# Optimization experiments

Hardware: AMD Instinct MI355X
Metric: run time of the kernel (lower is better)

Reference implementation:

```python
import jax, jax.numpy as jnp
import numpy as np

N, SD, HD, CD, AD = 8192, 64, 128, 32, 8  # num_agents, state_dim, hidden_dim, comm_dim, action_dim
NOISE_SCALE = 0.01


def _l2norm(x, axis):
    # F.normalize: x / max(||x||_2, eps), eps=1e-12
    return x / jnp.maximum(jnp.linalg.norm(x, axis=axis, keepdims=True), 1e-12)


def setup_inputs() -> dict:
    key = jax.random.key(0)
    ks = jax.random.split(key, 12)
    def w(k, shape, scale=0.05):
        return jax.random.normal(k, shape, jnp.float32) * scale
    return {
        "states": jax.random.normal(ks[0], (N, SD), jnp.float32),
        "noise": jax.random.normal(ks[1], (N, HD), jnp.float32),
        # ReasoningCore: Linear(SD+CD->HD), ReLU, Linear(HD->HD)
        "W1": w(ks[2], (SD + CD, HD)), "b1": jnp.zeros((HD,), jnp.float32),
        "W2": w(ks[3], (HD, HD)),      "b2": jnp.zeros((HD,), jnp.float32),
        # CommunicationModule encoder: Linear(HD->CD)
        "Wc": w(ks[4], (HD, CD)), "bc": jnp.zeros((CD,), jnp.float32),
        # GNNLayer: Linear(HD->HD)
        "Wg": w(ks[5], (HD, HD)), "bg": jnp.zeros((HD,), jnp.float32),
        # Policy: Linear(HD->AD)
        "Wp": w(ks[6], (HD, AD)), "bp": jnp.zeros((AD,), jnp.float32),
        # Value: Linear(HD->1)
        "Wv": w(ks[7], (HD, 1)), "bv": jnp.zeros((1,), jnp.float32),
        # RoleHead: Linear(HD->3)
        "Wr": w(ks[8], (HD, 3)), "br": jnp.zeros((3,), jnp.float32),
    }


def reference(states, noise, W1, b1, W2, b2, Wc, bc, Wg, bg, Wp, bp, Wv, bv, Wr, br):
    def core(x, comm):
        h = jax.nn.relu(jnp.concatenate([x, comm], axis=-1) @ W1 + b1)  # [N, HD]
        return h @ W2 + b2

    comm0 = jnp.zeros((N, CD), states.dtype)
    H = core(states, comm0)                                   # [N, HD]
    msgs = _l2norm(H @ Wc + bc, axis=1)                       # [N, CD]
    comm = jnp.broadcast_to(msgs.mean(axis=0, keepdims=True), (N, CD))
    H = core(states, comm)                                    # [N, HD]
    adj = jnp.ones((N, N), states.dtype) / N                  # dense uniform adjacency
    H = jax.nn.relu((adj @ H) @ Wg + bg)                      # GNN layer
    H = _l2norm(H + noise * NOISE_SCALE, axis=1)
    actions = jnp.tanh(H @ Wp + bp)                           # [N, AD]
    values = H @ Wv + bv                                      # [N, 1]
    role_probs = jax.nn.softmax(H @ Wr + br, axis=-1)         # [N, 3]
    return (H, actions, values, role_probs)
```

## Files before the change

kernel.cpp:

```cpp
#include <hip/hip_runtime.h>
#include <math.h>

#define N_AG 8192
#define SD 64
#define HD 128
#define CD 32
#define AD 8

#define P_OFF     0
#define W2CT_OFF  (N_AG*HD)
#define WALLT_OFF (W2CT_OFF + CD*HD)
#define BALL_OFF  (WALLT_OFF + 12*HD)
#define BCP_OFF   (BALL_OFF + 16)
#define MSUM_OFF  (BCP_OFF + CD)
#define HSUM_OFF  (MSUM_OFF + CD)

__global__ void k0_pre(const float* __restrict__ W2, const float* __restrict__ b2,
                       const float* __restrict__ Wc, const float* __restrict__ bc,
                       const float* __restrict__ Wp, const float* __restrict__ bp,
                       const float* __restrict__ Wv, const float* __restrict__ bv,
                       const float* __restrict__ Wr, const float* __restrict__ br,
                       float* __restrict__ ws) {
    int t = threadIdx.x, b = blockIdx.x;
    if (b < 16) {
        int idx = b * 256 + t;
        int c = idx & 31, k = idx >> 5;
        float s = 0.f;
        #pragma unroll 16
        for (int j = 0; j < HD; ++j) s += W2[k*HD + j] * Wc[j*CD + c];
        ws[W2CT_OFF + c*HD + k] = s;
    } else if (b == 16) {
        if (t < CD) {
            float s = bc[t];
            for (int j = 0; j < HD; ++j) s += b2[j] * Wc[j*CD + t];
            ws[BCP_OFF + t] = s;
            ws[MSUM_OFF + t] = 0.f;
        } else if (t >= 64 && t < 192) {
            ws[HSUM_OFF + t - 64] = 0.f;
        }
    } else {
        for (int idx = t; idx < 12 * HD; idx += 256) {
            int j = idx >> 7, k = idx & 127;
            float v = (j < 8) ? Wp[k*AD + j] : (j == 8) ? Wv[k] : Wr[k*3 + (j - 9)];
            ws[WALLT_OFF + idx] = v;
        }
        if (t < 12) ws[BALL_OFF + t] = (t < 8) ? bp[t] : (t == 8) ? bv[0] : br[t - 9];
    }
}

#define FMA4(acc, xv, w0, w1, w2, w3)                                   \
    acc.x += xv.x*w0.x + xv.y*w1.x + xv.z*w2.x + xv.w*w3.x;             \
    acc.y += xv.x*w0.y + xv.y*w1.y + xv.z*w2.y + xv.w*w3.y;             \
    acc.z += xv.x*w0.z + xv.y*w1.z + xv.z*w2.z + xv.w*w3.z;             \
    acc.w += xv.x*w0.w + xv.y*w1.w + xv.z*w2.w + xv.w*w3.w;

__global__ __launch_bounds__(256) void k1(const float* __restrict__ X,
                                          const float* __restrict__ W1,
                                          const float* __restrict__ b1,
                                          float* __restrict__ ws) {
    __shared__ float4 sX4[16][16];
    __shared__ float4 sT4[16][32];
    __shared__ float  sMg[16][32];
    int t = threadIdx.x;
    int a0 = blockIdx.x * 16;
    {
        int ag = t >> 4, k4 = t & 15;
        sX4[ag][k4] = ((const float4*)X)[(a0 + ag)*16 + k4];
    }
    __syncthreads();
    const int c4 = t & 31;
    const int A0 = t >> 5, A1 = A0 + 8;
    float4 bb = ((const float4*)b1)[c4];
    float4 acc0 = bb, acc1 = bb;
    #pragma unroll
    for (int k4 = 0; k4 < 16; ++k4) {
        float4 xA = sX4[A0][k4], xB = sX4[A1][k4];
        float4 w0 = ((const float4*)(W1 + (4*k4 + 0)*HD))[c4];
        float4 w1 = ((const float4*)(W1 + (4*k4 + 1)*HD))[c4];
        float4 w2 = ((const float4*)(W1 + (4*k4 + 2)*HD))[c4];
        float4 w3 = ((const float4*)(W1 + (4*k4 + 3)*HD))[c4];
        FMA4(acc0, xA, w0, w1, w2, w3);
        FMA4(acc1, xB, w0, w1, w2, w3);
    }
    ((float4*)(ws + P_OFF))[(a0 + A0)*32 + c4] = acc0;
    ((float4*)(ws + P_OFF))[(a0 + A1)*32 + c4] = acc1;
    float4 r0, r1;
    r0.x = fmaxf(acc0.x, 0.f); r0.y = fmaxf(acc0.y, 0.f); r0.z = fmaxf(acc0.z, 0.f); r0.w = fmaxf(acc0.w, 0.f);
    r1.x = fmaxf(acc1.x, 0.f); r1.y = fmaxf(acc1.y, 0.f); r1.z = fmaxf(acc1.z, 0.f); r1.w = fmaxf(acc1.w, 0.f);
    sT4[A0][c4] = r0;
    sT4[A1][c4] = r1;
    __syncthreads();
    float m0 = ws[BCP_OFF + c4], m1 = m0;
    const float4* w2cT = (const float4*)(ws + W2CT_OFF);
    #pragma unroll
    for (int k4 = 0; k4 < 32; ++k4) {
        float4 ta = sT4[A0][k4], tb = sT4[A1][k4];
        float4 wc = w2cT[c4*32 + k4];
        m0 += ta.x*wc.x + ta.y*wc.y + ta.z*wc.z + ta.w*wc.w;
        m1 += tb.x*wc.x + tb.y*wc.y + tb.z*wc.z + tb.w*wc.w;
    }
    float ss0 = m0*m0, ss1 = m1*m1;
    #pragma unroll
    for (int off = 1; off < 32; off <<= 1) {
        ss0 += __shfl_xor(ss0, off);
        ss1 += __shfl_xor(ss1, off);
    }
    float rv0 = 1.f / fmaxf(sqrtf(ss0), 1e-12f);
    float rv1 = 1.f / fmaxf(sqrtf(ss1), 1e-12f);
    sMg[A0][c4] = m0 * rv0;
    sMg[A1][c4] = m1 * rv1;
    __syncthreads();
    if (t < 32) {
        float s = 0.f;
        #pragma unroll
        for (int ag = 0; ag < 16; ++ag) s += sMg[ag][t];
        atomicAdd(&ws[MSUM_OFF + t], s);
    }
}

__global__ __launch_bounds__(256) void k2(const float* __restrict__ W1,
                                          float* __restrict__ ws) {
    __shared__ __align__(16) float sC[HD];
    __shared__ float4 sRed[8][32];
    int t = threadIdx.x;
    int a0 = blockIdx.x * 32;
    if (t < HD) {
        float s = 0.f;
        #pragma unroll
        for (int k = 0; k < CD; ++k) s += ws[MSUM_OFF + k] * W1[(SD + k)*HD + t];
        sC[t] = s * (1.f / (float)N_AG);
    }
    __syncthreads();
    const int c4 = t & 31, g = t >> 5;
    float4 cv = ((const float4*)sC)[c4];
    float4 acc; acc.x = acc.y = acc.z = acc.w = 0.f;
    #pragma unroll
    for (int i = 0; i < 4; ++i) {
        int ag = g + i*8;
        float4 p = ((const float4*)(ws + P_OFF))[(a0 + ag)*32 + c4];
        acc.x += fmaxf(p.x + cv.x, 0.f);
        acc.y += fmaxf(p.y + cv.y, 0.f);
        acc.z += fmaxf(p.z + cv.z, 0.f);
        acc.w += fmaxf(p.w + cv.w, 0.f);
    }
    sRed[g][c4] = acc;
    __syncthreads();
    if (t < 32) {
        float4 s = sRed[0][t];
        #pragma unroll
        for (int gg = 1; gg < 8; ++gg) {
            float4 v = sRed[gg][t];
            s.x += v.x; s.y += v.y; s.z += v.z; s.w += v.w;
        }
        atomicAdd(&ws[HSUM_OFF + 4*t + 0], s.x);
        atomicAdd(&ws[HSUM_OFF + 4*t + 1], s.y);
        atomicAdd(&ws[HSUM_OFF + 4*t + 2], s.z);
        atomicAdd(&ws[HSUM_OFF + 4*t + 3], s.w);
    }
}

__global__ __launch_bounds__(256) void k34(const float* __restrict__ noise,
                                           const float* __restrict__ W2, const float* __restrict__ b2,
                                           const float* __restrict__ Wg, const float* __restrict__ bg,
                                           float* __restrict__ ws, float* __restrict__ out) {
    __shared__ __align__(16) float sA[HD];
    __shared__ __align__(16) float sB[HD];
    __shared__ __align__(16) float sG[HD];
    __shared__ float4 sH4[16][32];
    int t = threadIdx.x;
    int a0 = blockIdx.x * 16;
    if (t < HD) sA[t] = ws[HSUM_OFF + t] * (1.f / (float)N_AG);
    __syncthreads();
    if (t < HD) {
        float s = b2[t];
        #pragma unroll 16
        for (int k = 0; k < HD; ++k) s += sA[k] * W2[k*HD + t];
        sB[t] = s;
    }
    __syncthreads();
    if (t < HD) {
        float s = bg[t];
        #pragma unroll 16
        for (int k = 0; k < HD; ++k) s += sB[k] * Wg[k*HD + t];
        sG[t] = fmaxf(s, 0.f);
    }
    __syncthreads();
    const int ag = t >> 4, q = t & 15;
    const int a = a0 + ag;
    float4 n0 = ((const float4*)noise)[a*32 + q*2];
    float4 n1 = ((const float4*)noise)[a*32 + q*2 + 1];
    float4 g0 = ((const float4*)sG)[q*2];
    float4 g1 = ((const float4*)sG)[q*2 + 1];
    float4 v0, v1;
    v0.x = g0.x + 0.01f*n0.x; v0.y = g0.y + 0.01f*n0.y; v0.z = g0.z + 0.01f*n0.z; v0.w = g0.w + 0.01f*n0.w;
    v1.x = g1.x + 0.01f*n1.x; v1.y = g1.y + 0.01f*n1.y; v1.z = g1.z + 0.01f*n1.z; v1.w = g1.w + 0.01f*n1.w;
    float ss = v0.x*v0.x + v0.y*v0.y + v0.z*v0.z + v0.w*v0.w
             + v1.x*v1.x + v1.y*v1.y + v1.z*v1.z + v1.w*v1.w;
    #pragma unroll
    for (int off = 1; off < 16; off <<= 1) ss += __shfl_xor(ss, off);
    float rinv = 1.f / fmaxf(sqrtf(ss), 1e-12f);
    float4 h0, h1;
    h0.x = v0.x*rinv; h0.y = v0.y*rinv; h0.z = v0.z*rinv; h0.w = v0.w*rinv;
    h1.x = v1.x*rinv; h1.y = v1.y*rinv; h1.z = v1.z*rinv; h1.w = v1.w*rinv;
    ((float4*)out)[a*32 + q*2]     = h0;
    ((float4*)out)[a*32 + q*2 + 1] = h1;
    sH4[ag][q*2]     = h0;
    sH4[ag][q*2 + 1] = h1;
    __syncthreads();
    float acc = 0.f;
    if (q < 12) {
        acc = ws[BALL_OFF + q];
        const float4* wT = (const float4*)(ws + WALLT_OFF);
        #pragma unroll
        for (int k4 = 0; k4 < 32; ++k4) {
            float4 hh = sH4[ag][k4];
            float4 w  = wT[q*32 + k4];
            acc += hh.x*w.x + hh.y*w.y + hh.z*w.z + hh.w*w.w;
        }
    }
    int base = (t & 63) & ~15;
    float a9  = __shfl(acc, base + 9, 64);
    float a10 = __shfl(acc, base + 10, 64);
    float a11 = __shfl(acc, base + 11, 64);
    float* outA = out + N_AG*HD;
    float* outV = outA + N_AG*AD;
    float* outR = outV + N_AG;
    if (q < 8) {
        outA[a*AD + q] = tanhf(acc);
    } else if (q == 8) {
        outV[a] = acc;
    } else if (q < 12) {
        float m = fmaxf(a9, fmaxf(a10, a11));
        float d = expf(a9 - m) + expf(a10 - m) + expf(a11 - m);
        outR[a*3 + (q - 9)] = expf(acc - m) / d;
    }
}

extern "C" void kernel_launch(void* const* d_in, const int* in_sizes, int n_in,
                              void* d_out, int out_size, void* d_ws, size_t ws_size,
                              hipStream_t stream) {
    const float* states = (const float*)d_in[0];
    const float* noise  = (const float*)d_in[1];
    const float* W1 = (const float*)d_in[2];
    const float* b1 = (const float*)d_in[3];
    const float* W2 = (const float*)d_in[4];
    const float* b2 = (const float*)d_in[5];
    const float* Wc = (const float*)d_in[6];
    const float* bc = (const float*)d_in[7];
    const float* Wg = (const float*)d_in[8];
    const float* bg = (const float*)d_in[9];
    const float* Wp = (const float*)d_in[10];
    const float* bp = (const float*)d_in[11];
    const float* Wv = (const float*)d_in[12];
    const float* bv = (const float*)d_in[13];
    const float* Wr = (const float*)d_in[14];
    const float* br = (const float*)d_in[15];
    float* ws  = (float*)d_ws;
    float* out = (float*)d_out;

    hipLaunchKernelGGL(k0_pre, dim3(18),  dim3(256), 0, stream,
                       W2, b2, Wc, bc, Wp, bp, Wv, bv, Wr, br, ws);
    hipLaunchKernelGGL(k1,     dim3(512), dim3(256), 0, stream, states, W1, b1, ws);
    hipLaunchKernelGGL(k2,     dim3(256), dim3(256), 0, stream, W1, ws);
    hipLaunchKernelGGL(k34,    dim3(512), dim3(256), 0, stream,
                       noise, W2, b2, Wg, bg, ws, out);
}
```

Measured before the change: 149.0 us.

## Drop precompute kernel; fuse weight prep into k1/k34, replace atomics with partials

Removes the k0_pre launch. k1 now computes the W2 and Wc matmuls directly instead of using a precomputed W2·Wc product, and writes per-block message partial sums rather than atomically adding them. k2 reduces those partials itself. k34 transposes the head weights into shared memory in every block. This saves one kernel launch and the atomic contention, at the cost of more FLOPs in k1 (a full HD×HD matmul per agent) and redundant weight staging in each k34 block.

Result: faster. 144.8 us (-2.8%).

```diff
diff --git a/kernel.cpp b/kernel.cpp
--- a/kernel.cpp
+++ b/kernel.cpp
@@ -6,47 +6,12 @@
 #define HD 128
 #define CD 32
 #define AD 8
+#define NB1 512
+#define NB2 256
 
 #define P_OFF     0
-#define W2CT_OFF  (N_AG*HD)
-#define WALLT_OFF (W2CT_OFF + CD*HD)
-#define BALL_OFF  (WALLT_OFF + 12*HD)
-#define BCP_OFF   (BALL_OFF + 16)
-#define MSUM_OFF  (BCP_OFF + CD)
-#define HSUM_OFF  (MSUM_OFF + CD)
-
-__global__ void k0_pre(const float* __restrict__ W2, const float* __restrict__ b2,
-                       const float* __restrict__ Wc, const float* __restrict__ bc,
-                       const float* __restrict__ Wp, const float* __restrict__ bp,
-                       const float* __restrict__ Wv, const float* __restrict__ bv,
-                       const float* __restrict__ Wr, const float* __restrict__ br,
-                       float* __restrict__ ws) {
-    int t = threadIdx.x, b = blockIdx.x;
-    if (b < 16) {
-        int idx = b * 256 + t;
-        int c = idx & 31, k = idx >> 5;
-        float s = 0.f;
-        #pragma unroll 16
-        for (int j = 0; j < HD; ++j) s += W2[k*HD + j] * Wc[j*CD + c];
-        ws[W2CT_OFF + c*HD + k] = s;
-    } else if (b == 16) {
-        if (t < CD) {
-            float s = bc[t];
-            for (int j = 0; j < HD; ++j) s += b2[j] * Wc[j*CD + t];
-            ws[BCP_OFF + t] = s;
-            ws[MSUM_OFF + t] = 0.f;
-        } else if (t >= 64 && t < 192) {
-            ws[HSUM_OFF + t - 64] = 0.f;
-        }
-    } else {
-        for (int idx = t; idx < 12 * HD; idx += 256) {
-            int j = idx >> 7, k = idx & 127;
-            float v = (j < 8) ? Wp[k*AD + j] : (j == 8) ? Wv[k] : Wr[k*3 + (j - 9)];
-            ws[WALLT_OFF + idx] = v;
-        }
-        if (t < 12) ws[BALL_OFF + t] = (t < 8) ? bp[t] : (t == 8) ? bv[0] : br[t - 9];
-    }
-}
+#define MPART_OFF (N_AG*HD)
+#define HSUM_OFF  (MPART_OFF + NB1*CD)
 
 #define FMA4(acc, xv, w0, w1, w2, w3)                                   \
     acc.x += xv.x*w0.x + xv.y*w1.x + xv.z*w2.x + xv.w*w3.x;             \
@@ -57,21 +22,22 @@
 __global__ __launch_bounds__(256) void k1(const float* __restrict__ X,
                                           const float* __restrict__ W1,
                                           const float* __restrict__ b1,
+                                          const float* __restrict__ W2,
+                                          const float* __restrict__ b2,
+                                          const float* __restrict__ Wc,
+                                          const float* __restrict__ bc,
                                           float* __restrict__ ws) {
     __shared__ float4 sX4[16][16];
     __shared__ float4 sT4[16][32];
-    __shared__ float  sMg[16][32];
-    int t = threadIdx.x;
-    int a0 = blockIdx.x * 16;
-    {
-        int ag = t >> 4, k4 = t & 15;
-        sX4[ag][k4] = ((const float4*)X)[(a0 + ag)*16 + k4];
-    }
-    __syncthreads();
-    const int c4 = t & 31;
-    const int A0 = t >> 5, A1 = A0 + 8;
+    __shared__ float4 sU4[16][32];
+    __shared__ float  sMg[16][CD];
+    int t = threadIdx.x, b = blockIdx.x, a0 = b * 16;
+    { int ag = t >> 4, k4 = t & 15; sX4[ag][k4] = ((const float4*)X)[(a0 + ag)*16 + k4]; }
+    if (b == 0 && t < HD) ws[HSUM_OFF + t] = 0.f;
+    __syncthreads();
+    const int c4 = t & 31, A0 = t >> 5, A1 = A0 + 8;
     float4 bb = ((const float4*)b1)[c4];
-    float4 acc0 = bb, acc1 = bb;
+    float4 p0 = bb, p1 = bb;
     #pragma unroll
     for (int k4 = 0; k4 < 16; ++k4) {
         float4 xA = sX4[A0][k4], xB = sX4[A1][k4];
@@ -79,25 +45,42 @@
         float4 w1 = ((const float4*)(W1 + (4*k4 + 1)*HD))[c4];
         float4 w2 = ((const float4*)(W1 + (4*k4 + 2)*HD))[c4];
         float4 w3 = ((const float4*)(W1 + (4*k4 + 3)*HD))[c4];
-        FMA4(acc0, xA, w0, w1, w2, w3);
-        FMA4(acc1, xB, w0, w1, w2, w3);
-    }
-    ((float4*)(ws + P_OFF))[(a0 + A0)*32 + c4] = acc0;
-    ((float4*)(ws + P_OFF))[(a0 + A1)*32 + c4] = acc1;
+        FMA4(p0, xA, w0, w1, w2, w3);
+        FMA4(p1, xB, w0, w1, w2, w3);
+    }
+    ((float4*)(ws + P_OFF))[(a0 + A0)*32 + c4] = p0;
+    ((float4*)(ws + P_OFF))[(a0 + A1)*32 + c4] = p1;
     float4 r0, r1;
-    r0.x = fmaxf(acc0.x, 0.f); r0.y = fmaxf(acc0.y, 0.f); r0.z = fmaxf(acc0.z, 0.f); r0.w = fmaxf(acc0.w, 0.f);
-    r1.x = fmaxf(acc1.x, 0.f); r1.y = fmaxf(acc1.y, 0.f); r1.z = fmaxf(acc1.z, 0.f); r1.w = fmaxf(acc1.w, 0.f);
+    r0.x = fmaxf(p0.x, 0.f); r0.y = fmaxf(p0.y, 0.f); r0.z = fmaxf(p0.z, 0.f); r0.w = fmaxf(p0.w, 0.f);
+    r1.x = fmaxf(p1.x, 0.f); r1.y = fmaxf(p1.y, 0.f); r1.z = fmaxf(p1.z, 0.f); r1.w = fmaxf(p1.w, 0.f);
     sT4[A0][c4] = r0;
     sT4[A1][c4] = r1;
     __syncthreads();
-    float m0 = ws[BCP_OFF + c4], m1 = m0;
-    const float4* w2cT = (const float4*)(ws + W2CT_OFF);
+    float4 b2v = ((const float4*)b2)[c4];
+    float4 u0 = b2v, u1 = b2v;
     #pragma unroll
     for (int k4 = 0; k4 < 32; ++k4) {
-        float4 ta = sT4[A0][k4], tb = sT4[A1][k4];
-        float4 wc = w2cT[c4*32 + k4];
-        m0 += ta.x*wc.x + ta.y*wc.y + ta.z*wc.z + ta.w*wc.w;
-        m1 += tb.x*wc.x + tb.y*wc.y + tb.z*wc.z + tb.w*wc.w;
+        float4 tA = sT4[A0][k4], tB = sT4[A1][k4];
+        float4 w0 = ((const float4*)(W2 + (4*k4 + 0)*HD))[c4];
+        float4 w1 = ((const float4*)(W2 + (4*k4 + 1)*HD))[c4];
+        float4 w2 = ((const float4*)(W2 + (4*k4 + 2)*HD))[c4];
+        float4 w3 = ((const float4*)(W2 + (4*k4 + 3)*HD))[c4];
+        FMA4(u0, tA, w0, w1, w2, w3);
+        FMA4(u1, tB, w0, w1, w2, w3);
+    }
+    sU4[A0][c4] = u0;
+    sU4[A1][c4] = u1;
+    __syncthreads();
+    float m0 = bc[c4], m1 = m0;
+    #pragma unroll 8
+    for (int k4 = 0; k4 < 32; ++k4) {
+        float4 uA = sU4[A0][k4], uB = sU4[A1][k4];
+        float w0 = Wc[(4*k4 + 0)*CD + c4];
+        float w1 = Wc[(4*k4 + 1)*CD + c4];
+        float w2 = Wc[(4*k4 + 2)*CD + c4];
+        float w3 = Wc[(4*k4 + 3)*CD + c4];
+        m0 += uA.x*w0 + uA.y*w1 + uA.z*w2 + uA.w*w3;
+        m1 += uB.x*w0 + uB.y*w1 + uB.z*w2 + uB.w*w3;
     }
     float ss0 = m0*m0, ss1 = m1*m1;
     #pragma unroll
@@ -105,29 +88,44 @@
         ss0 += __shfl_xor(ss0, off);
         ss1 += __shfl_xor(ss1, off);
     }
-    float rv0 = 1.f / fmaxf(sqrtf(ss0), 1e-12f);
-    float rv1 = 1.f / fmaxf(sqrtf(ss1), 1e-12f);
-    sMg[A0][c4] = m0 * rv0;
-    sMg[A1][c4] = m1 * rv1;
-    __syncthreads();
-    if (t < 32) {
+    sMg[A0][c4] = m0 * (1.f / fmaxf(sqrtf(ss0), 1e-12f));
+    sMg[A1][c4] = m1 * (1.f / fmaxf(sqrtf(ss1), 1e-12f));
+    __syncthreads();
+    if (t < CD) {
         float s = 0.f;
         #pragma unroll
         for (int ag = 0; ag < 16; ++ag) s += sMg[ag][t];
-        atomicAdd(&ws[MSUM_OFF + t], s);
+        ws[MPART_OFF + b*CD + t] = s;
     }
 }
 
 __global__ __launch_bounds__(256) void k2(const float* __restrict__ W1,
                                           float* __restrict__ ws) {
+    __shared__ float sPart[8][CD];
+    __shared__ float sMsum[CD];
     __shared__ __align__(16) float sC[HD];
     __shared__ float4 sRed[8][32];
     int t = threadIdx.x;
     int a0 = blockIdx.x * 32;
+    {
+        const int c = t & 31, chunk = t >> 5;
+        float s = 0.f;
+        for (int p = chunk*64; p < chunk*64 + 64; ++p)
+            s += ws[MPART_OFF + p*CD + c];
+        sPart[chunk][c] = s;
+    }
+    __syncthreads();
+    if (t < CD) {
+        float s = 0.f;
+        #pragma unroll
+        for (int j = 0; j < 8; ++j) s += sPart[j][t];
+        sMsum[t] = s;
+    }
+    __syncthreads();
     if (t < HD) {
         float s = 0.f;
         #pragma unroll
-        for (int k = 0; k < CD; ++k) s += ws[MSUM_OFF + k] * W1[(SD + k)*HD + t];
+        for (int k = 0; k < CD; ++k) s += sMsum[k] * W1[(SD + k)*HD + t];
         sC[t] = s * (1.f / (float)N_AG);
     }
     __syncthreads();
@@ -162,14 +160,24 @@
 __global__ __launch_bounds__(256) void k34(const float* __restrict__ noise,
                                            const float* __restrict__ W2, const float* __restrict__ b2,
                                            const float* __restrict__ Wg, const float* __restrict__ bg,
-                                           float* __restrict__ ws, float* __restrict__ out) {
+                                           const float* __restrict__ Wp, const float* __restrict__ bp,
+                                           const float* __restrict__ Wv, const float* __restrict__ bv,
+                                           const float* __restrict__ Wr, const float* __restrict__ br,
+                                           const float* __restrict__ ws, float* __restrict__ out) {
     __shared__ __align__(16) float sA[HD];
     __shared__ __align__(16) float sB[HD];
     __shared__ __align__(16) float sG[HD];
-    __shared__ float4 sH4[16][32];
+    __shared__ __align__(16) float sWT[12][HD + 4];
+    __shared__ float sBall[12];
+    __shared__ __align__(16) float4 sH4[16][33];
     int t = threadIdx.x;
     int a0 = blockIdx.x * 16;
-    if (t < HD) sA[t] = ws[HSUM_OFF + t] * (1.f / (float)N_AG);
+    for (int idx = t; idx < 12 * HD; idx += 256) {
+        int j = idx >> 7, k = idx & 127;
+        sWT[j][k] = (j < 8) ? Wp[k*AD + j] : (j == 8) ? Wv[k] : Wr[k*3 + (j - 9)];
+    }
+    if (t < 12) sBall[t] = (t < 8) ? bp[t] : (t == 8) ? bv[0] : br[t - 9];
+    if (t >= 64 && t < 64 + HD) sA[t - 64] = ws[HSUM_OFF + t - 64] * (1.f / (float)N_AG);
     __syncthreads();
     if (t < HD) {
         float s = b2[t];
@@ -209,12 +217,12 @@
     __syncthreads();
     float acc = 0.f;
     if (q < 12) {
-        acc = ws[BALL_OFF + q];
-        const float4* wT = (const float4*)(ws + WALLT_OFF);
+        acc = sBall[q];
+        const float4* wT = (const float4*)&sWT[q][0];
         #pragma unroll
         for (int k4 = 0; k4 < 32; ++k4) {
             float4 hh = sH4[ag][k4];
-            float4 w  = wT[q*32 + k4];
+            float4 w  = wT[k4];
             acc += hh.x*w.x + hh.y*w.y + hh.z*w.z + hh.w*w.w;
         }
     }
@@ -258,10 +266,9 @@
     float* ws  = (float*)d_ws;
     float* out = (float*)d_out;
 
-    hipLaunchKernelGGL(k0_pre, dim3(18),  dim3(256), 0, stream,
-                       W2, b2, Wc, bc, Wp, bp, Wv, bv, Wr, br, ws);
-    hipLaunchKernelGGL(k1,     dim3(512), dim3(256), 0, stream, states, W1, b1, ws);
-    hipLaunchKernelGGL(k2,     dim3(256), dim3(256), 0, stream, W1, ws);
-    hipLaunchKernelGGL(k34,    dim3(512), dim3(256), 0, stream,
-                       noise, W2, b2, Wg, bg, ws, out);
-}
+    hipLaunchKernelGGL(k1,  dim3(NB1), dim3(256), 0, stream,
+                       states, W1, b1, W2, b2, Wc, bc, ws);
+    hipLaunchKernelGGL(k2,  dim3(NB2), dim3(256), 0, stream, W1, ws);
+    hipLaunchKernelGGL(k34, dim3(NB1), dim3(256), 0, stream,
+                       noise, W2, b2, Wg, bg, Wp, bp, Wv, bv, Wr, br, ws, out);
+}
```
